# Kernel tuning notes

Measured on AMD Instinct MI355X. Metric: run time of the kernel, lower is better.

The kernel has to match this reference:

```python
import jax, jax.numpy as jnp
import numpy as np

D_MODEL = 768
D_STATE = 16
D_CONV = 4
EXPAND = 2
N_LAYERS = 8
VOCAB = 512
MAXSEQ = 2048
BATCH = 8
SEQ = 2048
D_INNER = EXPAND * D_MODEL
N_EMO, N_STY, N_KEY, N_MODE = 8, 8, 12, 2


def setup_inputs() -> dict:
    key = jax.random.key(0)
    ks = jax.random.split(key, 32)
    def nrm(k, shape, s=0.02):
        return (jax.random.normal(k, shape) * s).astype(jnp.float32)
    inp = {}
    inp['tokens'] = jax.random.randint(ks[0], (BATCH, SEQ), 0, VOCAB)
    inp['emotion'] = jax.random.randint(ks[1], (BATCH,), 0, N_EMO)
    inp['style'] = jax.random.randint(ks[2], (BATCH,), 0, N_STY)
    inp['key_sig'] = jax.random.randint(ks[3], (BATCH,), 0, N_KEY)
    inp['mode'] = jax.random.randint(ks[4], (BATCH,), 0, N_MODE)
    inp['bpm'] = (jax.random.uniform(ks[5], (BATCH,)) * 140.0 + 60.0).astype(jnp.float32)
    inp['tok_emb'] = nrm(ks[6], (VOCAB, D_MODEL))
    inp['emo_emb'] = nrm(ks[7], (N_EMO, D_MODEL))
    inp['sty_emb'] = nrm(ks[8], (N_STY, D_MODEL))
    inp['key_emb'] = nrm(ks[9], (N_KEY, D_MODEL))
    inp['mode_emb'] = nrm(ks[10], (N_MODE, D_MODEL))
    inp['bpm_w'] = nrm(ks[11], (D_MODEL, 1))
    inp['bpm_b'] = jnp.zeros((D_MODEL,), jnp.float32)
    inp['cond_w'] = nrm(ks[12], (D_MODEL, 5 * D_MODEL))
    inp['cond_b'] = jnp.zeros((D_MODEL,), jnp.float32)
    inp['pos_emb'] = nrm(ks[13], (MAXSEQ, D_MODEL))
    inp['ln_g'] = jnp.ones((N_LAYERS, D_MODEL), jnp.float32)
    inp['ln_b'] = jnp.zeros((N_LAYERS, D_MODEL), jnp.float32)
    inp['in_w'] = nrm(ks[14], (N_LAYERS, 2 * D_INNER, D_MODEL))
    inp['conv_w'] = nrm(ks[15], (N_LAYERS, D_INNER, 1, D_CONV), 0.1)
    inp['xproj_w'] = nrm(ks[16], (N_LAYERS, 2 * D_STATE, D_INNER))
    inp['dt_w'] = nrm(ks[17], (N_LAYERS, D_INNER, D_STATE))
    inp['dt_b'] = jnp.zeros((N_LAYERS, D_INNER), jnp.float32)
    inp['bproj_w'] = nrm(ks[18], (N_LAYERS, D_INNER, D_STATE))
    inp['d_param'] = jnp.ones((N_LAYERS, D_INNER), jnp.float32)
    inp['out_w'] = nrm(ks[19], (N_LAYERS, D_MODEL, D_INNER))
    inp['final_g'] = jnp.ones((D_MODEL,), jnp.float32)
    inp['final_b'] = jnp.zeros((D_MODEL,), jnp.float32)
    inp['head_w'] = nrm(ks[20], (VOCAB, D_MODEL))
    inp['head_b'] = jnp.zeros((VOCAB,), jnp.float32)
    return inp


def _layernorm(x, g, b):
    mu = x.mean(-1, keepdims=True)
    v = ((x - mu) ** 2).mean(-1, keepdims=True)
    return (x - mu) * jax.lax.rsqrt(v + 1e-5) * g + b


def _silu(x):
    return x * jax.nn.sigmoid(x)


def _mamba_block(x, in_w, conv_w, xproj_w, dt_w, dt_b, bproj_w, d_param, out_w):
    B, L, _ = x.shape
    xz = x @ in_w.T                       # [B,L,2*di]
    xc, z = jnp.split(xz, 2, axis=-1)
    # causal depthwise conv1d: torch pads d_conv-1 both sides then slices [:L]
    xt = jnp.transpose(xc, (0, 2, 1))     # [B,di,L]
    xt = jax.lax.conv_general_dilated(xt, conv_w, (1,), [(D_CONV - 1, 0)],
                                      feature_group_count=D_INNER)
    xc = _silu(jnp.transpose(xt, (0, 2, 1)))   # [B,L,di]
    dt_raw, b_raw = jnp.split(xc @ xproj_w.T, 2, axis=-1)  # each [B,L,ds]
    delta = jnp.clip(jax.nn.softplus(dt_raw @ dt_w.T + dt_b), 1e-4, 1.0)  # [B,L,di]
    bp = b_raw @ bproj_w.T                 # [B,L,di]

    def step(h, inputs):
        d, u, bb = inputs
        h = h * (1.0 - d) + u * bb
        return h, h

    xs = (jnp.transpose(delta, (1, 0, 2)),
          jnp.transpose(xc, (1, 0, 2)),
          jnp.transpose(bp, (1, 0, 2)))    # time-major [L,B,di]
    h0 = jnp.zeros((B, D_INNER), x.dtype)
    _, ys = jax.lax.scan(step, h0, xs)
    y = jnp.transpose(ys, (1, 0, 2)) + d_param * xc
    y = y * _silu(z)
    return y @ out_w.T


def reference(tokens, emotion, style, key_sig, mode, bpm, tok_emb, emo_emb, sty_emb,
              key_emb, mode_emb, bpm_w, bpm_b, cond_w, cond_b, pos_emb, ln_g, ln_b,
              in_w, conv_w, xproj_w, dt_w, dt_b, bproj_w, d_param, out_w,
              final_g, final_b, head_w, head_b):
    B, L = tokens.shape
    cond = jnp.concatenate([
        emo_emb[emotion], sty_emb[style], key_emb[key_sig], mode_emb[mode],
        bpm[:, None] @ bpm_w.T + bpm_b], axis=-1)       # [B,5d]
    cond = cond @ cond_w.T + cond_b                      # [B,d]
    x = tok_emb[tokens] + cond[:, None, :] + pos_emb[:L][None]
    for i in range(N_LAYERS):
        res = x
        h = _layernorm(x, ln_g[i], ln_b[i])
        x = res + _mamba_block(h, in_w[i], conv_w[i], xproj_w[i], dt_w[i],
                               dt_b[i], bproj_w[i], d_param[i], out_w[i])
    x = _layernorm(x, final_g, final_b)
    return x @ head_w.T + head_b
```

## Files before the change

kernel.cpp:

```cpp
#include <hip/hip_runtime.h>
#include <cstdint>

#define BATCH 8
#define SEQ   2048
#define DM    768
#define DI    1536
#define DS    16
#define NL    8
#define NVOCAB 512
#define BT    (BATCH*SEQ)
#define NCHUNK 32
#define TC    (SEQ/NCHUNK)

typedef __attribute__((ext_vector_type(8))) short bf16x8;
typedef __attribute__((ext_vector_type(4))) float f32x4;

__device__ __forceinline__ unsigned short f2bf(float f){
  unsigned int u = __float_as_uint(f);
  u += 0x7fffu + ((u >> 16) & 1u);
  return (unsigned short)(u >> 16);
}
__device__ __forceinline__ float bf2f(unsigned short s){
  return __uint_as_float(((unsigned int)s) << 16);
}
__device__ __forceinline__ float sigm(float x){ return 1.0f/(1.0f + __expf(-x)); }
__device__ __forceinline__ float siluf(float x){ return x * sigm(x); }
__device__ __forceinline__ float fast_softplus(float x){
  return (x > 15.0f) ? x : __logf(1.0f + __expf(x));
}
__device__ __forceinline__ void async16(void* l, const void* g){
  __builtin_amdgcn_global_load_lds(
      (const __attribute__((address_space(1))) unsigned int*)g,
      (__attribute__((address_space(3))) unsigned int*)l, 16, 0, 0);
}
__device__ __forceinline__ float dot4(f32x4 a, f32x4 b){
  return fmaf(a[0],b[0], fmaf(a[1],b[1], fmaf(a[2],b[2], a[3]*b[3])));
}

__global__ void cvt_bf16_kernel(const float4* __restrict__ in, ushort4* __restrict__ out, int n4){
  int i = blockIdx.x*256 + threadIdx.x;
  int stride = gridDim.x*256;
  for(; i<n4; i+=stride){
    float4 v = in[i];
    ushort4 o; o.x=f2bf(v.x); o.y=f2bf(v.y); o.z=f2bf(v.z); o.w=f2bf(v.w);
    out[i]=o;
  }
}

__global__ void wcomb_kernel(const float* __restrict__ dt_w, const float* __restrict__ bproj_w,
                             unsigned short* __restrict__ out){
  int idx = blockIdx.x*256 + threadIdx.x;
  int k = idx & 31, ld = idx >> 5;
  float v = (k < 16) ? dt_w[(long)ld*16 + k] : bproj_w[(long)ld*16 + (k-16)];
  out[idx] = f2bf(v);
}

__global__ __launch_bounds__(256) void cond_kernel(const int* __restrict__ emotion,
    const int* __restrict__ style, const int* __restrict__ keysig, const int* __restrict__ modei,
    const float* __restrict__ bpm, const float* __restrict__ emo_emb, const float* __restrict__ sty_emb,
    const float* __restrict__ key_emb, const float* __restrict__ mode_emb,
    const float* __restrict__ bpm_w, const float* __restrict__ bpm_b,
    const float* __restrict__ cond_w, const float* __restrict__ cond_b,
    float* __restrict__ cond_out){
  int b = blockIdx.y;
  int tid = threadIdx.x;
  __shared__ float vec[5*DM];
  int e = emotion[b], st = style[b], ks = keysig[b], md = modei[b];
  float bp = bpm[b];
  for(int j=tid; j<960; j+=256){
    int seg = j/192, o4 = j - seg*192;
    float4 v;
    if(seg==0)      v = reinterpret_cast<const float4*>(emo_emb + (long)e*DM)[o4];
    else if(seg==1) v = reinterpret_cast<const float4*>(sty_emb + (long)st*DM)[o4];
    else if(seg==2) v = reinterpret_cast<const float4*>(key_emb + (long)ks*DM)[o4];
    else if(seg==3) v = reinterpret_cast<const float4*>(mode_emb + (long)md*DM)[o4];
    else {
      float4 w = reinterpret_cast<const float4*>(bpm_w)[o4];
      float4 bb = reinterpret_cast<const float4*>(bpm_b)[o4];
      v = make_float4(fmaf(bp,w.x,bb.x), fmaf(bp,w.y,bb.y), fmaf(bp,w.z,bb.z), fmaf(bp,w.w,bb.w));
    }
    reinterpret_cast<float4*>(vec)[j] = v;
  }
  __syncthreads();
  int wid = tid>>6, lane = tid&63;
  int dm = blockIdx.x*4 + wid;
  const float4* w4 = reinterpret_cast<const float4*>(cond_w + (long)dm*(5*DM));
  const float4* v4 = reinterpret_cast<const float4*>(vec);
  float acc = 0.f;
  #pragma unroll 5
  for(int j=lane; j<960; j+=64){
    float4 w = w4[j], v = v4[j];
    acc = fmaf(w.x,v.x, fmaf(w.y,v.y, fmaf(w.z,v.z, fmaf(w.w,v.w, acc))));
  }
  #pragma unroll
  for(int off=32; off>0; off>>=1) acc += __shfl_xor(acc, off);
  if(lane==0) cond_out[b*DM + dm] = acc + cond_b[dm];
}

__global__ void embed_kernel(const int* __restrict__ tokens, const float* __restrict__ tok_emb,
    const float* __restrict__ cond, const float* __restrict__ pos_emb, float* __restrict__ x){
  int bt = blockIdx.x;
  int b = bt >> 11, t = bt & 2047;
  int tok = tokens[bt];
  const float4* te = reinterpret_cast<const float4*>(tok_emb + (long)tok*DM);
  const float4* ce = reinterpret_cast<const float4*>(cond + (long)b*DM);
  const float4* pe = reinterpret_cast<const float4*>(pos_emb + (long)t*DM);
  float4* xo = reinterpret_cast<float4*>(x + (long)bt*DM);
  int i = threadIdx.x;
  float4 a = te[i], c = ce[i], p = pe[i];
  xo[i] = make_float4(a.x+c.x+p.x, a.y+c.y+p.y, a.z+c.z+p.z, a.w+c.w+p.w);
}

__global__ __launch_bounds__(256) void ln_bf16_kernel(const float* __restrict__ x,
                     const float* __restrict__ g, const float* __restrict__ bta,
                     unsigned short* __restrict__ out){
  int row  = blockIdx.x*4 + (threadIdx.x >> 6);
  int lane = threadIdx.x & 63;
  const float* xr = x + (long)row*DM;
  float4 v[3];
  float sum=0.f, sq=0.f;
  #pragma unroll
  for(int i=0;i<3;i++){
    v[i] = *reinterpret_cast<const float4*>(xr + i*256 + lane*4);
    sum += v[i].x + v[i].y + v[i].z + v[i].w;
    sq  += v[i].x*v[i].x + v[i].y*v[i].y + v[i].z*v[i].z + v[i].w*v[i].w;
  }
  #pragma unroll
  for(int off=32; off>0; off>>=1){
    sum += __shfl_xor(sum, off);
    sq  += __shfl_xor(sq , off);
  }
  float mu  = sum * (1.0f/DM);
  float var = sq  * (1.0f/DM) - mu*mu;
  float rs  = rsqrtf(var + 1e-5f);
  unsigned short* orow = out + (long)row*DM;
  #pragma unroll
  for(int i=0;i<3;i++){
    int d = i*256 + lane*4;
    float4 gg = *reinterpret_cast<const float4*>(g + d);
    float4 bb = *reinterpret_cast<const float4*>(bta + d);
    ushort4 o;
    o.x = f2bf((v[i].x - mu)*rs*gg.x + bb.x);
    o.y = f2bf((v[i].y - mu)*rs*gg.y + bb.y);
    o.z = f2bf((v[i].z - mu)*rs*gg.z + bb.z);
    o.w = f2bf((v[i].w - mu)*rs*gg.w + bb.w);
    *reinterpret_cast<ushort4*>(orow + d) = o;
  }
}

template<int MODE>
__global__ __launch_bounds__(256) void gemm_lds(const unsigned short* __restrict__ A,
                                               const unsigned short* __restrict__ B,
                                               void* __restrict__ Cv,
                                               const float* __restrict__ bias,
                                               int K, int ldc){
  __shared__ short smem[2][2][128*64];
  const short* Ap = (const short*)A;
  const short* Bp = (const short*)B;
  int tid  = threadIdx.x;
  int lane = tid & 63;
  int wid  = tid >> 6;

  int nbx = gridDim.x;
  int id  = blockIdx.y*nbx + blockIdx.x;
  int q   = (nbx*gridDim.y) >> 3;
  int swz = (id & 7)*q + (id >> 3);
  int bx  = swz % nbx, by = swz / nbx;
  int row0 = by*128;
  int col0 = bx*128;

  int srow[4], goff[4];
  #pragma unroll
  for(int j=0;j<4;j++){
    int c = j*256 + tid;
    int row = c>>3, s = c&7;
    srow[j] = row;
    goff[j] = (s ^ (row&7))*8;
  }

  int wr = (wid>>1)*64;
  int wc = (wid&1)*64;
  int fr = lane & 15;
  int kq = lane >> 4;
  int fx = fr & 7;

  f32x4 acc[4][4];
  #pragma unroll
  for(int m=0;m<4;m++)
    #pragma unroll
    for(int n=0;n<4;n++)
      acc[m][n] = (f32x4){0.f,0.f,0.f,0.f};

  #define STAGE(buf, kt) { \
    char* aB = (char*)&smem[buf][0][0]; \
    char* bB = (char*)&smem[buf][1][0]; \
    _Pragma("unroll") \
    for(int j=0;j<4;j++){ \
      int c = j*256 + tid; \
      async16(aB + c*16, Ap + (long)(row0+srow[j])*K + (kt) + goff[j]); \
      async16(bB + c*16, Bp + (long)(col0+srow[j])*K + (kt) + goff[j]); \
    } }

  int NT = K >> 6;
  STAGE(0, 0)
  for(int t=0; t<NT; ++t){
    int cur = t & 1;
    if(t+1 < NT){
      STAGE(cur^1, (t+1)*64)
      asm volatile("s_waitcnt vmcnt(8)" ::: "memory");
    } else {
      asm volatile("s_waitcnt vmcnt(0)" ::: "memory");
    }
    __builtin_amdgcn_s_barrier();
    __builtin_amdgcn_sched_barrier(0);
    const short* As = &smem[cur][0][0];
    const short* Bs = &smem[cur][1][0];
    __builtin_amdgcn_s_setprio(1);
    #pragma unroll
    for(int ks=0; ks<2; ks++){
      int sA = ((ks*4 + kq) ^ fx) * 8;
      bf16x8 av[4], bv[4];
      #pragma unroll
      for(int m=0;m<4;m++)
        av[m] = *reinterpret_cast<const bf16x8*>(As + (wr + m*16 + fr)*64 + sA);
      #pragma unroll
      for(int n=0;n<4;n++)
        bv[n] = *reinterpret_cast<const bf16x8*>(Bs + (wc + n*16 + fr)*64 + sA);
      #pragma unroll
      for(int m=0;m<4;m++)
        #pragma unroll
        for(int n=0;n<4;n++)
          acc[m][n] = __builtin_amdgcn_mfma_f32_16x16x32_bf16(av[m], bv[n], acc[m][n], 0, 0, 0);
    }
    __builtin_amdgcn_s_setprio(0);
    __builtin_amdgcn_sched_barrier(0);
    __builtin_amdgcn_s_barrier();
  }
  #undef STAGE

  int rr = (lane >> 4) << 2;
  int cc = lane & 15;
  #pragma unroll
  for(int m=0;m<4;m++){
    #pragma unroll
    for(int n=0;n<4;n++){
      int col = col0 + wc + n*16 + cc;
      #pragma unroll
      for(int i=0;i<4;i++){
        long idx = (long)(row0 + wr + m*16 + rr + i)*ldc + col;
        float v = acc[m][n][i];
        if(MODE==3)      ((unsigned short*)Cv)[idx] = f2bf(v);
        else if(MODE==1) ((float*)Cv)[idx] += v;
        else if(MODE==2) ((float*)Cv)[idx] = v + bias[col];
        else             ((float*)Cv)[idx] = v;
      }
    }
  }
}

__global__ __launch_bounds__(256) void xproj_kernel(const unsigned short* __restrict__ xz,
      const float* __restrict__ cw, const unsigned short* __restrict__ wbf,
      float* __restrict__ dtb){
  __shared__ unsigned short xcs[16][DI+8];
  __shared__ float pdt[4][16][32];
  int blk = blockIdx.x;
  int b  = blk >> 7;
  int t0 = (blk & 127) << 4;
  int tid = threadIdx.x;
  long base = ((long)b*SEQ + t0)*(2*DI);
  if(tid < 192){
    int d0 = tid*8;
    float cc0[8], cc1[8], cc2[8], cc3[8];
    #pragma unroll
    for(int j=0;j<8;j++){
      cc0[j]=cw[(d0+j)*4+0]; cc1[j]=cw[(d0+j)*4+1];
      cc2[j]=cw[(d0+j)*4+2]; cc3[j]=cw[(d0+j)*4+3];
    }
    float wm3[8], wm2[8], wm1[8];
    #pragma unroll
    for(int j=0;j<8;j++){ wm3[j]=0.f; wm2[j]=0.f; wm1[j]=0.f; }
    if(t0>0){
      bf16x8 v3 = *reinterpret_cast<const bf16x8*>(xz + base - 3*(2*DI) + d0);
      bf16x8 v2 = *reinterpret_cast<const bf16x8*>(xz + base - 2*(2*DI) + d0);
      bf16x8 v1 = *reinterpret_cast<const bf16x8*>(xz + base - 1*(2*DI) + d0);
      #pragma unroll
      for(int j=0;j<8;j++){
        wm3[j]=bf2f((unsigned short)v3[j]);
        wm2[j]=bf2f((unsigned short)v2[j]);
        wm1[j]=bf2f((unsigned short)v1[j]);
      }
    }
    for(int tt=0; tt<16; tt++){
      bf16x8 vt = *reinterpret_cast<const bf16x8*>(xz + base + (long)tt*(2*DI) + d0);
      bf16x8 o;
      #pragma unroll
      for(int j=0;j<8;j++){
        float wt = bf2f((unsigned short)vt[j]);
        float u  = cc0[j]*wm3[j] + cc1[j]*wm2[j] + cc2[j]*wm1[j] + cc3[j]*wt;
        o[j] = (short)f2bf(siluf(u));
        wm3[j]=wm2[j]; wm2[j]=wm1[j]; wm1[j]=wt;
      }
      *reinterpret_cast<bf16x8*>(&xcs[tt][d0]) = o;
    }
  }
  __syncthreads();
  int wid = tid >> 6, lane = tid & 63;
  int fr = lane & 15, kq = lane >> 4;
  f32x4 a0 = (f32x4){0.f,0.f,0.f,0.f};
  f32x4 a1 = (f32x4){0.f,0.f,0.f,0.f};
  const unsigned short* w0 = wbf + (long)fr*DI;
  const unsigned short* w1 = wbf + (long)(16+fr)*DI;
  int kbase = wid*384 + kq*8;
  #pragma unroll
  for(int ks=0; ks<12; ks++){
    int k = kbase + ks*32;
    bf16x8 av = *reinterpret_cast<const bf16x8*>(&xcs[fr][k]);
    bf16x8 b0 = *reinterpret_cast<const bf16x8*>(w0 + k);
    bf16x8 b1 = *reinterpret_cast<const bf16x8*>(w1 + k);
    a0 = __builtin_amdgcn_mfma_f32_16x16x32_bf16(av, b0, a0, 0, 0, 0);
    a1 = __builtin_amdgcn_mfma_f32_16x16x32_bf16(av, b1, a1, 0, 0, 0);
  }
  int rr = kq << 2;
  #pragma unroll
  for(int i=0;i<4;i++){
    pdt[wid][rr+i][fr]      = a0[i];
    pdt[wid][rr+i][16+fr]   = a1[i];
  }
  __syncthreads();
  for(int e = tid; e < 512; e += 256){
    int r = e >> 5, s = e & 31;
    float v = pdt[0][r][s] + pdt[1][r][s] + pdt[2][r][s] + pdt[3][r][s];
    dtb[((long)b*SEQ + t0 + r)*32 + s] = v;
  }
}

__global__ __launch_bounds__(256) void scanAY_mfma_kernel(const unsigned short* __restrict__ xz,
      const float* __restrict__ dtb, const float* __restrict__ cw,
      const unsigned short* __restrict__ wcomb,
      const float* __restrict__ dtbias_g, const float* __restrict__ dp_g,
      float2* __restrict__ chunk, unsigned short* __restrict__ y0s,
      unsigned short* __restrict__ as_s){
  __shared__ unsigned short abuf[64][32];
  __shared__ unsigned short dab[64*256*2];
  int c = blockIdx.x, db = blockIdx.y, b = blockIdx.z;
  int tid = threadIdx.x;
  int t0 = c*TC;
  {
    const float4* src = reinterpret_cast<const float4*>(dtb + ((long)b*SEQ + t0)*32);
    float4 v0 = src[tid*2], v1 = src[tid*2+1];
    bf16x8 o;
    o[0]=(short)f2bf(v0.x); o[1]=(short)f2bf(v0.y); o[2]=(short)f2bf(v0.z); o[3]=(short)f2bf(v0.w);
    o[4]=(short)f2bf(v1.x); o[5]=(short)f2bf(v1.y); o[6]=(short)f2bf(v1.z); o[7]=(short)f2bf(v1.w);
    *reinterpret_cast<bf16x8*>(&abuf[tid>>2][(tid&3)*8]) = o;
  }
  __syncthreads();
  {
    int w = tid >> 6, lane = tid & 63;
    int fr = lane & 15, kq = lane >> 4;
    bf16x8 zero = {0,0,0,0,0,0,0,0};
    bf16x8 bq[4], bp[4];
    #pragma unroll
    for(int nt=0; nt<4; nt++){
      int dcol = db*256 + w*64 + nt*16 + fr;
      bf16x8 wv = *reinterpret_cast<const bf16x8*>(wcomb + (long)dcol*32 + kq*8);
      bq[nt] = (kq<2) ? wv : zero;
      bp[nt] = (kq<2) ? zero : wv;
    }
    #pragma unroll
    for(int mt=0; mt<4; mt++){
      bf16x8 av = *reinterpret_cast<const bf16x8*>(&abuf[mt*16 + fr][kq*8]);
      #pragma unroll
      for(int nt=0; nt<4; nt++){
        f32x4 aq = __builtin_amdgcn_mfma_f32_16x16x32_bf16(av, bq[nt], (f32x4){0.f,0.f,0.f,0.f}, 0,0,0);
        f32x4 ap = __builtin_amdgcn_mfma_f32_16x16x32_bf16(av, bp[nt], (f32x4){0.f,0.f,0.f,0.f}, 0,0,0);
        int dl = w*64 + nt*16 + fr;
        #pragma unroll
        for(int i=0;i<4;i++){
          int t = mt*16 + kq*4 + i;
          unsigned int pack = (unsigned int)f2bf(aq[i]) | (((unsigned int)f2bf(ap[i]))<<16);
          *reinterpret_cast<unsigned int*>(&dab[(t*256 + dl)*2]) = pack;
        }
      }
    }
  }
  int d = db*256 + tid;
  float c0=cw[d*4],c1=cw[d*4+1],c2=cw[d*4+2],c3=cw[d*4+3];
  float bias = dtbias_g[d];
  float dp = dp_g[d];
  asm volatile("" : "+v"(c0),"+v"(c1),"+v"(c2),"+v"(c3),"+v"(bias),"+v"(dp));
  long base = ((long)b*SEQ + t0)*(2*DI) + d;
  float wm3 = (t0>0) ? bf2f(xz[base - 3*(2*DI)]) : 0.f;
  float wm2 = (t0>0) ? bf2f(xz[base - 2*(2*DI)]) : 0.f;
  float wm1 = (t0>0) ? bf2f(xz[base - 1*(2*DI)]) : 0.f;
  const unsigned short* xp = xz + base;
  long sidx = ((long)b*SEQ + t0)*DI + d;
  unsigned short* yp = y0s + sidx;
  unsigned short* ap2 = as_s + sidx;
  __syncthreads();
  float h = 0.f, P = 1.f;
  const unsigned int* dab32 = reinterpret_cast<const unsigned int*>(dab);
  for(int g=0; g<TC/8; g++){
    unsigned short xv[8];
    #pragma unroll
    for(int j=0;j<8;j++){ xv[j] = xp[(long)j*2*DI]; }
    xp += 8L*2*DI;
    #pragma unroll
    for(int j=0;j<8;j++){
      float wt = bf2f(xv[j]);
      float u = siluf(fmaf(c3,wt, fmaf(c2,wm1, fmaf(c1,wm2, c0*wm3))));
      wm3=wm2; wm2=wm1; wm1=wt;
      unsigned int pk = dab32[(g*8+j)*256 + tid];
      float da = bias + bf2f((unsigned short)(pk & 0xffffu));
      float ba = bf2f((unsigned short)(pk >> 16));
      float delta = fminf(fmaxf(fast_softplus(da), 1e-4f), 1.0f);
      float a = 1.0f - delta;
      h = fmaf(h, a, u*ba);
      P *= a;
      yp[(long)j*DI]  = f2bf(fmaf(dp, u, h));
      ap2[(long)j*DI] = f2bf(P);
    }
    yp += 8L*DI; ap2 += 8L*DI;
  }
  chunk[((long)b*DI + d)*NCHUNK + c] = make_float2(P, h);
}

__global__ __launch_bounds__(256) void scanAY_kernel(const unsigned short* __restrict__ xz,
      const float* __restrict__ dtb, const float* __restrict__ cw,
      const float* __restrict__ dtw_g, const float* __restrict__ dtbias_g,
      const float* __restrict__ bpw_g, const float* __restrict__ dp_g,
      float2* __restrict__ chunk, unsigned short* __restrict__ y,
      unsigned short* __restrict__ asz_s){
  __shared__ float dsb[TC*32];
  int c = blockIdx.x, db = blockIdx.y, b = blockIdx.z;
  int d = db*256 + threadIdx.x;
  int t0 = c*TC;
  {
    const float4* src = reinterpret_cast<const float4*>(dtb + ((long)b*SEQ + t0)*32);
    float4* dst = reinterpret_cast<float4*>(dsb);
    dst[threadIdx.x]       = src[threadIdx.x];
    dst[threadIdx.x + 256] = src[threadIdx.x + 256];
  }
  float c0=cw[d*4],c1=cw[d*4+1],c2=cw[d*4+2],c3=cw[d*4+3];
  f32x4 wq0 = *reinterpret_cast<const f32x4*>(dtw_g + d*16 + 0);
  f32x4 wq1 = *reinterpret_cast<const f32x4*>(dtw_g + d*16 + 4);
  f32x4 wq2 = *reinterpret_cast<const f32x4*>(dtw_g + d*16 + 8);
  f32x4 wq3 = *reinterpret_cast<const f32x4*>(dtw_g + d*16 + 12);
  f32x4 wp0 = *reinterpret_cast<const f32x4*>(bpw_g + d*16 + 0);
  f32x4 wp1 = *reinterpret_cast<const f32x4*>(bpw_g + d*16 + 4);
  f32x4 wp2 = *reinterpret_cast<const f32x4*>(bpw_g + d*16 + 8);
  f32x4 wp3 = *reinterpret_cast<const f32x4*>(bpw_g + d*16 + 12);
  float bias = dtbias_g[d];
  float dp = dp_g[d];
  asm volatile("" : "+v"(wq0),"+v"(wq1),"+v"(wq2),"+v"(wq3),
                    "+v"(wp0),"+v"(wp1),"+v"(wp2),"+v"(wp3),
                    "+v"(c0),"+v"(c1),"+v"(c2),"+v"(c3),"+v"(bias),"+v"(dp));
  long base = ((long)b*SEQ + t0)*(2*DI) + d;
  float wm3 = (t0>0) ? bf2f(xz[base - 3*(2*DI)]) : 0.f;
  float wm2 = (t0>0) ? bf2f(xz[base - 2*(2*DI)]) : 0.f;
  float wm1 = (t0>0) ? bf2f(xz[base - 1*(2*DI)]) : 0.f;
  const unsigned short* xp = xz + base;
  const unsigned short* zp = xz + base + DI;
  long sidx = ((long)b*SEQ + t0)*DI + d;
  unsigned short* yp = y + sidx;
  unsigned short* ap = asz_s + sidx;
  __syncthreads();
  float h = 0.f, P = 1.f;
  for(int g=0; g<TC/8; g++){
    unsigned short xv[8], zv[8];
    #pragma unroll
    for(int j=0;j<8;j++){ xv[j] = xp[(long)j*2*DI]; zv[j] = zp[(long)j*2*DI]; }
    xp += 8L*2*DI; zp += 8L*2*DI;
    const float* rp = dsb + g*8*32;
    #pragma unroll
    for(int j=0;j<8;j++){
      float wt = bf2f(xv[j]);
      float u = siluf(fmaf(c3,wt, fmaf(c2,wm1, fmaf(c1,wm2, c0*wm3))));
      wm3=wm2; wm2=wm1; wm1=wt;
      const f32x4* row = reinterpret_cast<const f32x4*>(rp + j*32);
      float da = bias + dot4(row[0],wq0) + dot4(row[1],wq1) + dot4(row[2],wq2) + dot4(row[3],wq3);
      float ba =        dot4(row[4],wp0) + dot4(row[5],wp1) + dot4(row[6],wp2) + dot4(row[7],wp3);
      float delta = fminf(fmaxf(fast_softplus(da), 1e-4f), 1.0f);
      float a = 1.0f - delta;
      h = fmaf(h, a, u*ba);
      P *= a;
      float sz = siluf(bf2f(zv[j]));
      yp[(long)j*DI] = f2bf(fmaf(dp, u, h) * sz);
      ap[(long)j*DI] = f2bf(P * sz);
    }
    yp += 8L*DI; ap += 8L*DI;
  }
  chunk[((long)b*DI + d)*NCHUNK + c] = make_float2(P, h);
}

__global__ __launch_bounds__(256) void h0_kernel(const float2* __restrict__ chunk,
                                                 float* __restrict__ h0tab){
  int idx = blockIdx.x*256 + threadIdx.x;
  int b = idx / DI, d = idx - b*DI;
  const float2* cb = chunk + ((long)b*DI + d)*NCHUNK;
  float h0 = 0.f;
  for(int c=0; c<NCHUNK; c++){
    h0tab[((long)b*NCHUNK + c)*DI + d] = h0;
    float2 ps = cb[c];
    h0 = fmaf(ps.x, h0, ps.y);
  }
}

__global__ __launch_bounds__(256) void fixup_z_kernel(const unsigned short* __restrict__ as_s,
      const float* __restrict__ h0tab, const unsigned short* __restrict__ xz,
      unsigned short* __restrict__ y){
  int i = (blockIdx.x*256 + threadIdx.x)*8;
  int bt = i / DI;
  int d  = i - bt*DI;
  int b  = bt >> 11;
  int c  = (bt & 2047) >> 6;
  const float* hp = h0tab + ((long)b*NCHUNK + c)*DI + d;
  f32x4 h0a = *reinterpret_cast<const f32x4*>(hp);
  f32x4 h0b = *reinterpret_cast<const f32x4*>(hp + 4);
  bf16x8 yv = *reinterpret_cast<const bf16x8*>(y + i);
  bf16x8 av = *reinterpret_cast<const bf16x8*>(as_s + i);
  bf16x8 zv = *reinterpret_cast<const bf16x8*>(xz + (long)bt*(2*DI) + DI + d);
  bf16x8 o;
  #pragma unroll
  for(int j=0;j<8;j++){
    float h0 = (j<4) ? h0a[j] : h0b[j-4];
    float v = fmaf(h0, bf2f((unsigned short)av[j]), bf2f((unsigned short)yv[j]));
    o[j] = (short)f2bf(v * siluf(bf2f((unsigned short)zv[j])));
  }
  *reinterpret_cast<bf16x8*>(y + i) = o;
}

__global__ __launch_bounds__(256) void fixup_kernel(const unsigned short* __restrict__ asz_s,
      const float* __restrict__ h0tab, unsigned short* __restrict__ y){
  int i = (blockIdx.x*256 + threadIdx.x)*8;
  int bt = i / DI;
  int d  = i - bt*DI;
  int b  = bt >> 11;
  int c  = (bt & 2047) >> 6;
  const float* hp = h0tab + ((long)b*NCHUNK + c)*DI + d;
  f32x4 h0a = *reinterpret_cast<const f32x4*>(hp);
  f32x4 h0b = *reinterpret_cast<const f32x4*>(hp + 4);
  bf16x8 yv = *reinterpret_cast<const bf16x8*>(y + i);
  bf16x8 av = *reinterpret_cast<const bf16x8*>(asz_s + i);
  bf16x8 o;
  #pragma unroll
  for(int j=0;j<8;j++){
    float h0 = (j<4) ? h0a[j] : h0b[j-4];
    o[j] = (short)f2bf(fmaf(h0, bf2f((unsigned short)av[j]), bf2f((unsigned short)yv[j])));
  }
  *reinterpret_cast<bf16x8*>(y + i) = o;
}

extern "C" void kernel_launch(void* const* d_in, const int* in_sizes, int n_in,
                              void* d_out, int out_size, void* d_ws, size_t ws_size,
                              hipStream_t stream){
  const int*   tokens  = (const int*)  d_in[0];
  const int*   emotion = (const int*)  d_in[1];
  const int*   style   = (const int*)  d_in[2];
  const int*   keysig  = (const int*)  d_in[3];
  const int*   modei   = (const int*)  d_in[4];
  const float* bpm     = (const float*)d_in[5];
  const float* tok_emb = (const float*)d_in[6];
  const float* emo_emb = (const float*)d_in[7];
  const float* sty_emb = (const float*)d_in[8];
  const float* key_emb = (const float*)d_in[9];
  const float* mode_emb= (const float*)d_in[10];
  const float* bpm_w   = (const float*)d_in[11];
  const float* bpm_b   = (const float*)d_in[12];
  const float* cond_w  = (const float*)d_in[13];
  const float* cond_b  = (const float*)d_in[14];
  const float* pos_emb = (const float*)d_in[15];
  const float* ln_g    = (const float*)d_in[16];
  const float* ln_b    = (const float*)d_in[17];
  const float* in_w    = (const float*)d_in[18];
  const float* conv_w  = (const float*)d_in[19];
  const float* xproj_w = (const float*)d_in[20];
  const float* dt_w    = (const float*)d_in[21];
  const float* dt_b    = (const float*)d_in[22];
  const float* bproj_w = (const float*)d_in[23];
  const float* d_param = (const float*)d_in[24];
  const float* out_w   = (const float*)d_in[25];
  const float* final_g = (const float*)d_in[26];
  const float* final_b = (const float*)d_in[27];
  const float* head_w  = (const float*)d_in[28];
  const float* head_b  = (const float*)d_in[29];

  char* ws = (char*)d_ws;
  float*          x       = (float*)(ws + 0L);
  unsigned short* hy      = (unsigned short*)(ws + 50331648L);
  unsigned short* xz      = (unsigned short*)(ws + 100663296L);
  float*          dtbuf   = (float*)(ws + 201326592L);
  float2*         chunk   = (float2*)(ws + 203423744L);
  float*          condv   = (float*)(ws + 206569472L);
  unsigned short* inwb    = (unsigned short*)(ws + 206594048L);
  unsigned short* outwb   = (unsigned short*)(ws + 211312640L);
  unsigned short* headwb  = (unsigned short*)(ws + 213671936L);
  unsigned short* wbf_all = (unsigned short*)(ws + 214458368L);
  float*          h0tab   = (float*)(ws + 215244800L);
  unsigned short* asz_s   = (unsigned short*)(ws + 216817664L);
  unsigned short* wcombb  = (unsigned short*)(ws + 267149312L);

  const bool use_y0   = (ws_size >= 267149312UL);
  const bool use_mfma = (ws_size >= 267935744UL);

  unsigned short* h_bf = hy;
  unsigned short* y_bf = hy;
  unsigned short* xfin = hy;

  cvt_bf16_kernel<<<128,256,0,stream>>>((const float4*)head_w,(ushort4*)headwb, NVOCAB*DM/4);
  cvt_bf16_kernel<<<384,256,0,stream>>>((const float4*)xproj_w,(ushort4*)wbf_all, NL*32*DI/4);
  if(use_mfma)
    wcomb_kernel<<<NL*DI*32/256,256,0,stream>>>(dt_w, bproj_w, wcombb);
  cond_kernel<<<dim3(DM/4,8),256,0,stream>>>(emotion, style, keysig, modei, bpm, emo_emb, sty_emb,
        key_emb, mode_emb, bpm_w, bpm_b, cond_w, cond_b, condv);
  embed_kernel<<<BT,192,0,stream>>>(tokens, tok_emb, condv, pos_emb, x);

  for(int l=0; l<NL; l++){
    cvt_bf16_kernel<<<1024,256,0,stream>>>((const float4*)(in_w  + (long)l*2*DI*DM), (ushort4*)inwb,  2*DI*DM/4);
    cvt_bf16_kernel<<<512, 256,0,stream>>>((const float4*)(out_w + (long)l*DM*DI),   (ushort4*)outwb, DM*DI/4);
    ln_bf16_kernel<<<BT/4,256,0,stream>>>(x, ln_g + l*DM, ln_b + l*DM, h_bf);
    gemm_lds<3><<<dim3(2*DI/128, BT/128),256,0,stream>>>(h_bf, inwb, xz, nullptr, DM, 2*DI);
    xproj_kernel<<<BT/16,256,0,stream>>>(xz, conv_w + l*DI*4, wbf_all + (long)l*32*DI, dtbuf);
    if(use_mfma){
      scanAY_mfma_kernel<<<dim3(NCHUNK,6,BATCH),256,0,stream>>>(xz, dtbuf, conv_w + l*DI*4,
            wcombb + (long)l*DI*32, dt_b + l*DI, d_param + l*DI, chunk, y_bf, asz_s);
      h0_kernel<<<48,256,0,stream>>>(chunk, h0tab);
      fixup_z_kernel<<<BT*DI/(256*8),256,0,stream>>>(asz_s, h0tab, xz, y_bf);
    } else {
      scanAY_kernel<<<dim3(NCHUNK,6,BATCH),256,0,stream>>>(xz, dtbuf, conv_w + l*DI*4,
            dt_w + l*DI*DS, dt_b + l*DI, bproj_w + l*DI*DS, d_param + l*DI, chunk, y_bf, asz_s);
      h0_kernel<<<48,256,0,stream>>>(chunk, h0tab);
      fixup_kernel<<<BT*DI/(256*8),256,0,stream>>>(asz_s, h0tab, y_bf);
    }
    gemm_lds<1><<<dim3(DM/128, BT/128),256,0,stream>>>(y_bf, outwb, x, nullptr, DI, DM);
  }
  ln_bf16_kernel<<<BT/4,256,0,stream>>>(x, final_g, final_b, xfin);
  gemm_lds<2><<<dim3(NVOCAB/128, BT/128),256,0,stream>>>(xfin, headwb, d_out, head_b, DM, NVOCAB);
}
```

Measured before the change: 2.467 ms.

## Add 256x256 tile GEMM for in_proj and simplify gemm_lds to single buffer

Introduces a 512-thread, 256x256-tile double-buffered MFMA GEMM used for the in_proj projection, increasing operand reuse per LDS load and reducing global traffic. The generic gemm_lds kernel is changed to a single-buffered loop with __syncthreads, halving its LDS footprint but removing load/compute overlap for the out_proj and head GEMMs. The large tile uses 128KB of LDS per block, limiting occupancy to one block per CU.

```diff
diff --git a/kernel.cpp b/kernel.cpp
--- a/kernel.cpp
+++ b/kernel.cpp
@@ -154,7 +154,8 @@
                                                void* __restrict__ Cv,
                                                const float* __restrict__ bias,
                                                int K, int ldc){
-  __shared__ short smem[2][2][128*64];
+  __shared__ short As[128*64];
+  __shared__ short Bs[128*64];
   const short* Ap = (const short*)A;
   const short* Bp = (const short*)B;
   int tid  = threadIdx.x;
@@ -191,31 +192,14 @@
     for(int n=0;n<4;n++)
       acc[m][n] = (f32x4){0.f,0.f,0.f,0.f};
 
-  #define STAGE(buf, kt) { \
-    char* aB = (char*)&smem[buf][0][0]; \
-    char* bB = (char*)&smem[buf][1][0]; \
-    _Pragma("unroll") \
-    for(int j=0;j<4;j++){ \
-      int c = j*256 + tid; \
-      async16(aB + c*16, Ap + (long)(row0+srow[j])*K + (kt) + goff[j]); \
-      async16(bB + c*16, Bp + (long)(col0+srow[j])*K + (kt) + goff[j]); \
-    } }
-
-  int NT = K >> 6;
-  STAGE(0, 0)
-  for(int t=0; t<NT; ++t){
-    int cur = t & 1;
-    if(t+1 < NT){
-      STAGE(cur^1, (t+1)*64)
-      asm volatile("s_waitcnt vmcnt(8)" ::: "memory");
-    } else {
-      asm volatile("s_waitcnt vmcnt(0)" ::: "memory");
-    }
-    __builtin_amdgcn_s_barrier();
-    __builtin_amdgcn_sched_barrier(0);
-    const short* As = &smem[cur][0][0];
-    const short* Bs = &smem[cur][1][0];
-    __builtin_amdgcn_s_setprio(1);
+  for(int kt=0; kt<K; kt+=64){
+    #pragma unroll
+    for(int j=0;j<4;j++){
+      int c = j*256 + tid;
+      async16((char*)As + c*16, Ap + (long)(row0+srow[j])*K + kt + goff[j]);
+      async16((char*)Bs + c*16, Bp + (long)(col0+srow[j])*K + kt + goff[j]);
+    }
+    __syncthreads();
     #pragma unroll
     for(int ks=0; ks<2; ks++){
       int sA = ((ks*4 + kq) ^ fx) * 8;
@@ -232,11 +216,8 @@
         for(int n=0;n<4;n++)
           acc[m][n] = __builtin_amdgcn_mfma_f32_16x16x32_bf16(av[m], bv[n], acc[m][n], 0, 0, 0);
     }
-    __builtin_amdgcn_s_setprio(0);
-    __builtin_amdgcn_sched_barrier(0);
-    __builtin_amdgcn_s_barrier();
-  }
-  #undef STAGE
+    __syncthreads();
+  }
 
   int rr = (lane >> 4) << 2;
   int cc = lane & 15;
@@ -253,6 +234,117 @@
         else if(MODE==1) ((float*)Cv)[idx] += v;
         else if(MODE==2) ((float*)Cv)[idx] = v + bias[col];
         else             ((float*)Cv)[idx] = v;
+      }
+    }
+  }
+}
+
+__global__ __launch_bounds__(512) void gemm256(const unsigned short* __restrict__ A,
+                                               const unsigned short* __restrict__ B,
+                                               unsigned short* __restrict__ C,
+                                               int K, int ldc){
+  __shared__ short smem[2][2][256*64];
+  const short* Ap = (const short*)A;
+  const short* Bp = (const short*)B;
+  int tid  = threadIdx.x;
+  int lane = tid & 63;
+  int wid  = tid >> 6;
+
+  int nbx = gridDim.x;
+  int id  = blockIdx.y*nbx + blockIdx.x;
+  int q   = (nbx*gridDim.y) >> 3;
+  int swz = (id & 7)*q + (id >> 3);
+  int bx  = swz % nbx, by = swz / nbx;
+  int row0 = by*256;
+  int col0 = bx*256;
+
+  int srow[4], goff[4];
+  #pragma unroll
+  for(int j=0;j<4;j++){
+    int c = j*512 + tid;
+    int row = c>>3, s = c&7;
+    srow[j] = row;
+    goff[j] = (s ^ (row&7))*8;
+  }
+
+  int wr = (wid>>2)*128;
+  int wc = (wid&3)*64;
+  int fr = lane & 15;
+  int kq = lane >> 4;
+  int fx = fr & 7;
+
+  f32x4 acc[8][4];
+  #pragma unroll
+  for(int m=0;m<8;m++)
+    #pragma unroll
+    for(int n=0;n<4;n++)
+      acc[m][n] = (f32x4){0.f,0.f,0.f,0.f};
+
+  #define STAGE256(buf, kt) { \
+    char* aB = (char*)&smem[buf][0][0]; \
+    char* bB = (char*)&smem[buf][1][0]; \
+    _Pragma("unroll") \
+    for(int j=0;j<4;j++){ \
+      int c = j*512 + tid; \
+      async16(aB + c*16, Ap + (long)(row0+srow[j])*K + (kt) + goff[j]); \
+      async16(bB + c*16, Bp + (long)(col0+srow[j])*K + (kt) + goff[j]); \
+    } }
+
+  int NT = K >> 6;
+  STAGE256(0, 0)
+  for(int t=0; t<NT; ++t){
+    int cur = t & 1;
+    if(t+1 < NT){
+      STAGE256(cur^1, (t+1)*64)
+      asm volatile("s_waitcnt vmcnt(8)" ::: "memory");
+    } else {
+      asm volatile("s_waitcnt vmcnt(0)" ::: "memory");
+    }
+    __builtin_amdgcn_s_barrier();
+    __builtin_amdgcn_sched_barrier(0);
+    const short* As = &smem[cur][0][0];
+    const short* Bs = &smem[cur][1][0];
+    __builtin_amdgcn_s_setprio(1);
+    #pragma unroll
+    for(int qp=0; qp<4; qp++){
+      int qm = qp>>1, qn = qp&1;
+      bf16x8 av[4][2], bv[2][2];
+      #pragma unroll
+      for(int ks=0; ks<2; ks++){
+        int sA = ((ks*4 + kq) ^ fx) * 8;
+        #pragma unroll
+        for(int m4=0;m4<4;m4++)
+          av[m4][ks] = *reinterpret_cast<const bf16x8*>(As + (wr + (qm*4+m4)*16 + fr)*64 + sA);
+        #pragma unroll
+        for(int n2=0;n2<2;n2++)
+          bv[n2][ks] = *reinterpret_cast<const bf16x8*>(Bs + (wc + (qn*2+n2)*16 + fr)*64 + sA);
+      }
+      #pragma unroll
+      for(int ks=0; ks<2; ks++)
+        #pragma unroll
+        for(int m4=0;m4<4;m4++)
+          #pragma unroll
+          for(int n2=0;n2<2;n2++)
+            acc[qm*4+m4][qn*2+n2] = __builtin_amdgcn_mfma_f32_16x16x32_bf16(
+                av[m4][ks], bv[n2][ks], acc[qm*4+m4][qn*2+n2], 0, 0, 0);
+    }
+    __builtin_amdgcn_s_setprio(0);
+    __builtin_amdgcn_sched_barrier(0);
+    __builtin_amdgcn_s_barrier();
+  }
+  #undef STAGE256
+
+  int rr = (lane >> 4) << 2;
+  int cc = lane & 15;
+  #pragma unroll
+  for(int m=0;m<8;m++){
+    #pragma unroll
+    for(int n=0;n<4;n++){
+      int col = col0 + wc + n*16 + cc;
+      #pragma unroll
+      for(int i=0;i<4;i++){
+        long idx = (long)(row0 + wr + m*16 + rr + i)*ldc + col;
+        C[idx] = f2bf(acc[m][n][i]);
       }
     }
   }
@@ -599,7 +691,6 @@
   unsigned short* asz_s   = (unsigned short*)(ws + 216817664L);
   unsigned short* wcombb  = (unsigned short*)(ws + 267149312L);
 
-  const bool use_y0   = (ws_size >= 267149312UL);
   const bool use_mfma = (ws_size >= 267935744UL);
 
   unsigned short* h_bf = hy;
@@ -618,7 +709,7 @@
     cvt_bf16_kernel<<<1024,256,0,stream>>>((const float4*)(in_w  + (long)l*2*DI*DM), (ushort4*)inwb,  2*DI*DM/4);
     cvt_bf16_kernel<<<512, 256,0,stream>>>((const float4*)(out_w + (long)l*DM*DI),   (ushort4*)outwb, DM*DI/4);
     ln_bf16_kernel<<<BT/4,256,0,stream>>>(x, ln_g + l*DM, ln_b + l*DM, h_bf);
-    gemm_lds<3><<<dim3(2*DI/128, BT/128),256,0,stream>>>(h_bf, inwb, xz, nullptr, DM, 2*DI);
+    gemm256<<<dim3(2*DI/256, BT/256),512,0,stream>>>(h_bf, inwb, xz, DM, 2*DI);
     xproj_kernel<<<BT/16,256,0,stream>>>(xz, conv_w + l*DI*4, wbf_all + (long)l*32*DI, dtbuf);
     if(use_mfma){
       scanAY_mfma_kernel<<<dim3(NCHUNK,6,BATCH),256,0,stream>>>(xz, dtbuf, conv_w + l*DI*4,
```

Measured after the change: 2.307 ms. -6.5%, faster.
